# Optimization experiments

Measured on AMD Instinct MI355X. Metric: run time of the kernel, lower is better.

## Reference

```python
import jax, jax.numpy as jnp
import numpy as np

IN_FEATURES = 4096
OUT_FEATURES = 4096
GROUP_SIZE = 128


def _unpack_int4_last_dim(packed):
    # packed: [..., P] int32 -> [..., P*8] int32 nibbles in [0,15]
    shifts = jnp.arange(0, 32, 4, dtype=jnp.int32)
    u = (packed[..., None] >> shifts) & 15
    return u.reshape(*packed.shape[:-1], packed.shape[-1] * 8)


def setup_inputs() -> dict:
    key = jax.random.key(0)
    k1, k2, k3, k4, k5 = jax.random.split(key, 5)
    groups = IN_FEATURES // GROUP_SIZE  # 32
    x = jax.random.normal(k1, (4096, IN_FEATURES), dtype=jnp.float32)
    qweight = jax.random.randint(k2, (OUT_FEATURES, IN_FEATURES // 8), 0, 2147483647, dtype=jnp.int32)
    qzeros = jax.random.randint(k3, (OUT_FEATURES, groups // 8), 0, 2147483647, dtype=jnp.int32)
    scales = jax.random.uniform(k4, (OUT_FEATURES, groups), dtype=jnp.float32) * 0.02 + 0.001
    bias = jax.random.normal(k5, (OUT_FEATURES,), dtype=jnp.float32)
    return {"x": x, "qweight": qweight, "qzeros": qzeros, "scales": scales, "bias": bias}


def _dequantize_weight(qweight, qzeros, scales):
    # qweight: [out, in/8] -> w_int: [out, in]
    w_int = _unpack_int4_last_dim(qweight).astype(jnp.float32)
    # qzeros: [out, groups/8] -> zeros: [out, groups]
    zeros = _unpack_int4_last_dim(qzeros).astype(jnp.float32)
    group_ids = jnp.arange(IN_FEATURES) // GROUP_SIZE  # [in]
    # expand per-group scale/zero along in_features
    w = (w_int - zeros[:, group_ids]) * scales[:, group_ids]  # [out, in]
    return w


def reference(x, qweight, qzeros, scales, bias):
    w = _dequantize_weight(qweight, qzeros, scales)  # [out, in] fp32
    return x @ w.T + bias  # [tokens, out]
```

## Files before the change

### kernel.cpp

```cpp
#include <hip/hip_runtime.h>
#include <hip/hip_bf16.h>

#define TOKENS 4096
#define IN_F   4096
#define OUT_F  4096

typedef __bf16 bf16x8 __attribute__((ext_vector_type(8)));
typedef float  f32x4  __attribute__((ext_vector_type(4)));
typedef unsigned int u32;
typedef u32 u32x4 __attribute__((ext_vector_type(4)));

#define DEQ_BLOCKS 2048
#define CVT_BLOCKS 4096

__device__ __forceinline__ void gld_lds16(const void* g, void* l) {
    __builtin_amdgcn_global_load_lds(
        (const __attribute__((address_space(1))) u32*)g,
        (__attribute__((address_space(3))) u32*)l,
        16, 0, 0);
}

__global__ __launch_bounds__(256) void prep_kernel(
        const u32* __restrict__ qweight, const u32* __restrict__ qzeros,
        const float* __restrict__ scales, const float* __restrict__ x,
        __bf16* __restrict__ W, __bf16* __restrict__ A) {
    const int tid = threadIdx.x;
    if (blockIdx.x < DEQ_BLOCKS) {
        int idx4 = blockIdx.x * 256 + tid;
        int n  = idx4 >> 7;
        int p4 = (idx4 & 127) << 2;
        int g  = p4 >> 4;
        u32 qz = qzeros[(n << 2) + (g >> 3)];
        float z = (float)((qz >> ((g & 7) * 4)) & 15);
        float s = scales[(n << 5) + g];
        u32x4 qw = *(const u32x4*)(qweight + (size_t)n * 512 + p4);
        __bf16* dst = W + (size_t)n * IN_F + p4 * 8;
#pragma unroll
        for (int c = 0; c < 4; ++c) {
            bf16x8 h;
#pragma unroll
            for (int j = 0; j < 8; ++j) {
                float w = ((float)((qw[c] >> (4 * j)) & 15) - z) * s;
                h[j] = (__bf16)w;
            }
            *(bf16x8*)(dst + c * 8) = h;
        }
    } else {
        int idx = (blockIdx.x - DEQ_BLOCKS) * 256 + tid;
        const f32x4* xp = (const f32x4*)x + (size_t)idx * 4;
        f32x4 v0 = xp[0], v1 = xp[1], v2 = xp[2], v3 = xp[3];
        bf16x8 h0, h1;
#pragma unroll
        for (int j = 0; j < 4; ++j) {
            h0[j] = (__bf16)v0[j]; h0[4 + j] = (__bf16)v1[j];
            h1[j] = (__bf16)v2[j]; h1[4 + j] = (__bf16)v3[j];
        }
        bf16x8* ap = (bf16x8*)A + (size_t)idx * 2;
        ap[0] = h0; ap[1] = h1;
    }
}

__global__ __launch_bounds__(256, 4) void gemm_bt(
        const __bf16* __restrict__ A, const __bf16* __restrict__ B,
        const float* __restrict__ bias, float* __restrict__ C) {
    __shared__ __align__(16) __bf16 lsA[128 * 64];
    __shared__ __align__(16) __bf16 lsB[128 * 64];

    const int t    = threadIdx.x;
    const int bm   = blockIdx.y, bn = blockIdx.x;
    const int lane = t & 63, wave = t >> 6;
    const int wm   = (wave >> 1) * 64;
    const int wn   = (wave & 1) * 64;
    const int lr   = lane & 15;
    const int quad = lane >> 4;

    const __bf16* Abase = A + (size_t)bm * 128 * IN_F;
    const __bf16* Bbase = B + (size_t)bn * 128 * IN_F;

    int srow[4], scol[4];
#pragma unroll
    for (int u = 0; u < 4; ++u) {
        int q = t + u * 256;
        srow[u] = q >> 3;
        scol[u] = ((q & 7) ^ ((q >> 3) & 7)) * 8;
    }

    f32x4 acc[4][4] = {};

    for (int k0 = 0; k0 < IN_F; k0 += 64) {
#pragma unroll
        for (int u = 0; u < 4; ++u) {
            int q = t + u * 256;
            gld_lds16(Abase + (size_t)srow[u] * IN_F + k0 + scol[u],
                      (char*)lsA + q * 16);
            gld_lds16(Bbase + (size_t)srow[u] * IN_F + k0 + scol[u],
                      (char*)lsB + q * 16);
        }
        __syncthreads();

#pragma unroll
        for (int sub = 0; sub < 2; ++sub) {
            bf16x8 af[4], bf[4];
#pragma unroll
            for (int i = 0; i < 4; ++i) {
                const int Ra = wm + i * 16 + lr;
                const int Rb = wn + i * 16 + lr;
                const int ca = ((sub * 4 + quad) ^ (Ra & 7)) * 8;
                const int cb = ((sub * 4 + quad) ^ (Rb & 7)) * 8;
                af[i] = *(const bf16x8*)(lsA + Ra * 64 + ca);
                bf[i] = *(const bf16x8*)(lsB + Rb * 64 + cb);
            }
#pragma unroll
            for (int i = 0; i < 4; ++i)
#pragma unroll
                for (int j = 0; j < 4; ++j)
                    acc[i][j] = __builtin_amdgcn_mfma_f32_16x16x32_bf16(
                        af[i], bf[j], acc[i][j], 0, 0, 0);
        }
        __syncthreads();
    }

    const int row0 = bm * 128 + wm + quad * 4;
    const int col0 = bn * 128 + wn + lr;
#pragma unroll
    for (int j = 0; j < 4; ++j) {
        const int col = col0 + j * 16;
        const float bv = bias[col];
#pragma unroll
        for (int i = 0; i < 4; ++i) {
            const int row = row0 + i * 16;
#pragma unroll
            for (int r = 0; r < 4; ++r)
                C[(size_t)(row + r) * OUT_F + col] = acc[i][j][r] + bv;
        }
    }
}

extern "C" void kernel_launch(void* const* d_in, const int* in_sizes, int n_in,
                              void* d_out, int out_size, void* d_ws, size_t ws_size,
                              hipStream_t stream) {
    (void)in_sizes; (void)n_in; (void)out_size; (void)ws_size;
    const float* x       = (const float*)d_in[0];
    const u32*   qweight = (const u32*)d_in[1];
    const u32*   qzeros  = (const u32*)d_in[2];
    const float* scales  = (const float*)d_in[3];
    const float* bias    = (const float*)d_in[4];
    float* out = (float*)d_out;

    __bf16* W   = (__bf16*)d_ws;
    __bf16* Abf = (__bf16*)((char*)d_ws + (size_t)OUT_F * IN_F * 2);

    prep_kernel<<<dim3(DEQ_BLOCKS + CVT_BLOCKS), dim3(256), 0, stream>>>(
        qweight, qzeros, scales, x, W, Abf);
    gemm_bt<<<dim3(OUT_F / 128, TOKENS / 128), dim3(256), 0, stream>>>(
        Abf, W, bias, out);
}
```

Baseline: 255.4 us.

## Rewrite GEMM as 256x256 tile, 8-wave ping-pong pipelined kernel

The GEMM is replaced with a 512-thread kernel that computes a 256x256 output tile per block. Global-to-LDS loads are double-buffered and interleaved with MFMA phases using explicit barriers, vmcnt waits and s_setprio. Block IDs are remapped for better L2 locality and the LDS swizzle is changed. The intent is to hide load latency and raise arithmetic intensity per block, at the cost of 128KB LDS per block and more accumulator registers. Occupancy drops and the schedule depends on hand-placed waits being correct.

```diff
diff --git a/kernel.cpp b/kernel.cpp
--- a/kernel.cpp
+++ b/kernel.cpp
@@ -60,74 +60,116 @@
     }
 }
 
-__global__ __launch_bounds__(256, 4) void gemm_bt(
+__global__ __launch_bounds__(512, 2) void gemm8p(
         const __bf16* __restrict__ A, const __bf16* __restrict__ B,
         const float* __restrict__ bias, float* __restrict__ C) {
-    __shared__ __align__(16) __bf16 lsA[128 * 64];
-    __shared__ __align__(16) __bf16 lsB[128 * 64];
+    __shared__ __align__(16) char lsA[65536];
+    __shared__ __align__(16) char lsB[65536];
 
     const int t    = threadIdx.x;
-    const int bm   = blockIdx.y, bn = blockIdx.x;
     const int lane = t & 63, wave = t >> 6;
-    const int wm   = (wave >> 1) * 64;
-    const int wn   = (wave & 1) * 64;
-    const int lr   = lane & 15;
-    const int quad = lane >> 4;
+    const int lr   = lane & 15, quad = lane >> 4;
+    const int wm   = (wave >> 2) * 128;
+    const int wn   = (wave & 3) * 64;
 
-    const __bf16* Abase = A + (size_t)bm * 128 * IN_F;
-    const __bf16* Bbase = B + (size_t)bn * 128 * IN_F;
+    int bid = blockIdx.x;
+    bid = (bid & 7) * 32 + (bid >> 3);
+    const int bm = bid >> 4, bn = bid & 15;
 
-    int srow[4], scol[4];
-#pragma unroll
-    for (int u = 0; u < 4; ++u) {
-        int q = t + u * 256;
-        srow[u] = q >> 3;
-        scol[u] = ((q & 7) ^ ((q >> 3) & 7)) * 8;
+    const __bf16* Abase = A + (size_t)bm * 256 * IN_F;
+    const __bf16* Bbase = B + (size_t)bn * 256 * IN_F;
+
+    const int srow0 = t >> 2;
+    const int srow1 = 128 + (t >> 2);
+    const int scol0 = ((t & 3) ^ ((srow0 >> 1) & 3)) * 8;
+    const int scol1 = ((t & 3) ^ ((srow1 >> 1) & 3)) * 8;
+
+#define STAGE(OPBASE, LS, KT, KH, BUF) do {                                  \
+    int _kb = (((KT) & 63) * 64 + (KH) * 32);                                \
+    gld_lds16(OPBASE + (size_t)srow0 * IN_F + _kb + scol0,                   \
+              LS + ((BUF) * 2 + (KH)) * 16384 + t * 16);                     \
+    gld_lds16(OPBASE + (size_t)srow1 * IN_F + _kb + scol1,                   \
+              LS + ((BUF) * 2 + (KH)) * 16384 + 8192 + t * 16);              \
+} while (0)
+
+    bf16x8 af[4], bfr[4];
+    f32x4 acc[8][4] = {};
+
+#define LDA4(PM, KH, BUF) do {                                               \
+    _Pragma("unroll")                                                        \
+    for (int i = 0; i < 4; ++i) {                                            \
+        const int R = wm + (PM) * 64 + i * 16 + lr;                          \
+        af[i] = *(const bf16x8*)(lsA + ((BUF) * 2 + (KH)) * 16384 +          \
+                                 R * 64 + ((quad ^ ((R >> 1) & 3)) * 16));   \
+    }                                                                        \
+} while (0)
+
+#define LDB4(KH, BUF) do {                                                   \
+    _Pragma("unroll")                                                        \
+    for (int j = 0; j < 4; ++j) {                                            \
+        const int R = wn + j * 16 + lr;                                      \
+        bfr[j] = *(const bf16x8*)(lsB + ((BUF) * 2 + (KH)) * 16384 +         \
+                                  R * 64 + ((quad ^ ((R >> 1) & 3)) * 16));  \
+    }                                                                        \
+} while (0)
+
+#define MFMA16(PM) do {                                                      \
+    _Pragma("unroll")                                                        \
+    for (int i = 0; i < 4; ++i)                                              \
+    _Pragma("unroll")                                                        \
+    for (int j = 0; j < 4; ++j)                                              \
+        acc[(PM) * 4 + i][j] = __builtin_amdgcn_mfma_f32_16x16x32_bf16(      \
+            af[i], bfr[j], acc[(PM) * 4 + i][j], 0, 0, 0);                   \
+} while (0)
+
+#define FENCE() asm volatile("" ::: "memory")
+#define BAR()  do { FENCE(); __builtin_amdgcn_s_barrier(); FENCE(); } while (0)
+#define VM8()  asm volatile("s_waitcnt vmcnt(8)" ::: "memory")
+#define PRIO(x) __builtin_amdgcn_s_setprio(x)
+
+    STAGE(Abase, lsA, 0, 0, 0);
+    STAGE(Bbase, lsB, 0, 0, 0);
+    STAGE(Abase, lsA, 0, 1, 0);
+    STAGE(Bbase, lsB, 0, 1, 0);
+    STAGE(Abase, lsA, 1, 0, 1);
+    STAGE(Bbase, lsB, 1, 0, 1);
+    VM8();
+    BAR();
+
+#define TILE(KT, B) do {                                                     \
+       \
+    LDB4(0, B); LDA4(0, 0, B);                                               \
+    STAGE(Abase, lsA, (KT) + 1, 1, 1 - (B));                                 \
+    BAR(); PRIO(1); MFMA16(0); PRIO(0); BAR();                               \
+                        \
+    LDA4(1, 0, B);                                                           \
+    STAGE(Bbase, lsB, (KT) + 1, 1, 1 - (B));                                 \
+    BAR(); PRIO(1); MFMA16(1); PRIO(0); VM8(); BAR();                        \
+        \
+    LDB4(1, B); LDA4(0, 1, B);                                               \
+    STAGE(Abase, lsA, (KT) + 2, 0, B);                                       \
+    BAR(); PRIO(1); MFMA16(0); PRIO(0); BAR();                               \
+                                         \
+    LDA4(1, 1, B);                                                           \
+    STAGE(Bbase, lsB, (KT) + 2, 0, B);                                       \
+    BAR(); PRIO(1); MFMA16(1); PRIO(0); VM8(); BAR();                        \
+} while (0)
+
+    for (int kt = 0; kt < 64; kt += 2) {
+        TILE(kt, 0);
+        TILE(kt + 1, 1);
     }
 
-    f32x4 acc[4][4] = {};
+    asm volatile("s_waitcnt vmcnt(0)" ::: "memory");
 
-    for (int k0 = 0; k0 < IN_F; k0 += 64) {
-#pragma unroll
-        for (int u = 0; u < 4; ++u) {
-            int q = t + u * 256;
-            gld_lds16(Abase + (size_t)srow[u] * IN_F + k0 + scol[u],
-                      (char*)lsA + q * 16);
-            gld_lds16(Bbase + (size_t)srow[u] * IN_F + k0 + scol[u],
-                      (char*)lsB + q * 16);
-        }
-        __syncthreads();
-
-#pragma unroll
-        for (int sub = 0; sub < 2; ++sub) {
-            bf16x8 af[4], bf[4];
-#pragma unroll
-            for (int i = 0; i < 4; ++i) {
-                const int Ra = wm + i * 16 + lr;
-                const int Rb = wn + i * 16 + lr;
-                const int ca = ((sub * 4 + quad) ^ (Ra & 7)) * 8;
-                const int cb = ((sub * 4 + quad) ^ (Rb & 7)) * 8;
-                af[i] = *(const bf16x8*)(lsA + Ra * 64 + ca);
-                bf[i] = *(const bf16x8*)(lsB + Rb * 64 + cb);
-            }
-#pragma unroll
-            for (int i = 0; i < 4; ++i)
-#pragma unroll
-                for (int j = 0; j < 4; ++j)
-                    acc[i][j] = __builtin_amdgcn_mfma_f32_16x16x32_bf16(
-                        af[i], bf[j], acc[i][j], 0, 0, 0);
-        }
-        __syncthreads();
-    }
-
-    const int row0 = bm * 128 + wm + quad * 4;
-    const int col0 = bn * 128 + wn + lr;
+    const int row0 = bm * 256 + wm + quad * 4;
+    const int col0 = bn * 256 + wn + lr;
 #pragma unroll
     for (int j = 0; j < 4; ++j) {
         const int col = col0 + j * 16;
         const float bv = bias[col];
 #pragma unroll
-        for (int i = 0; i < 4; ++i) {
+        for (int i = 0; i < 8; ++i) {
             const int row = row0 + i * 16;
 #pragma unroll
             for (int r = 0; r < 4; ++r)
@@ -152,6 +194,5 @@
 
     prep_kernel<<<dim3(DEQ_BLOCKS + CVT_BLOCKS), dim3(256), 0, stream>>>(
         qweight, qzeros, scales, x, W, Abf);
-    gemm_bt<<<dim3(OUT_F / 128, TOKENS / 128), dim3(256), 0, stream>>>(
-        Abf, W, bias, out);
+    gemm8p<<<dim3(256), dim3(512), 0, stream>>>(Abf, W, bias, out);
 }
```

Result: no change. 257.8 us (+0.9%).
